# Performance work log

Measured on AMD Instinct MI355X. Metric: run time of the kernel, lower is better.

Reference implementation:

```python
import jax, jax.numpy as jnp
import numpy as np

NUM_HEADS = 12
HEAD_SIZE = 64
B1, B2 = 28, 52          # get_block_sizes(use_dynamic=False): (1456//52, 52)
NUM_FRAMES = 2
SEQ = NUM_FRAMES * B1 * B2   # 2912
BATCH = 1
SCALE = HEAD_SIZE ** -0.5


def _rope(x, cos, sin):
    # interleaved rotary (is_neox_style=False); x [B,T,H,D], cos/sin [T,D//2]
    x1, x2 = x[..., 0::2], x[..., 1::2]
    c, s = cos[:, None, :], sin[:, None, :]
    o1 = x1 * c - x2 * s
    o2 = x2 * c + x1 * s
    return jnp.stack([o1, o2], axis=-1).reshape(x.shape)


def _blin(x, W, b):
    # per-head (batched replicated) linear: x [..., H, Din], W [H, Dout, Din], b [H, Dout]
    return jnp.einsum('...hd,hed->...he', x, W) + b


def _sdpa(q, k, v):
    # q [N,1,H,D], k/v [N,L,H,D] -> [N,1,H,D]
    s = jnp.einsum('nqhd,nkhd->nhqk', q, k) * SCALE
    p = jax.nn.softmax(s, axis=-1)
    return jnp.einsum('nhqk,nkhd->nqhd', p, v)


def _forward(lq, lk, rq, rk, v, cos, sin,
             W_lkq, b_lkq, W_lkk, b_lkk, W_lkv, b_lkv,
             W_rqq, b_rqq, W_rqk, b_rqk, W_rqv, b_rqv):
    B, S, H, D = lq.shape
    F = S // (B1 * B2)
    hd2 = D // 2
    lq_r = _rope(lq, cos, sin).reshape(B, F, B1, B2, H, D)
    # ---- left factor: local attention over b2 within each (frame, b1) block ----
    lkq = lk.reshape(B, F, B1, B2, H, D)[:, :, :, 0]           # [B,F,B1,H,D]
    lkq = _blin(lkq, W_lkq, b_lkq)
    cos_k = cos.reshape(F, B1, B2, hd2)[:, :, 0].reshape(F * B1, hd2)
    sin_k = sin.reshape(F, B1, B2, hd2)[:, :, 0].reshape(F * B1, hd2)
    lkq = _rope(lkq.reshape(B, F * B1, H, D), cos_k, sin_k).reshape(B, F, B1, H, D)
    lkk = _rope(_blin(lk, W_lkk, b_lkk), cos, sin).reshape(B, F, B1, B2, H, D)
    lkv = _blin(lk, W_lkv, b_lkv).reshape(B, F, B1, B2, H, D)
    x = _sdpa(lkq.reshape(-1, 1, H, D), lkk.reshape(-1, B2, H, D), lkv.reshape(-1, B2, H, D))
    lk_out = _rope(x.reshape(B, F * B1, H, D), cos_k, sin_k).reshape(B, F, B1, H, D)
    L = jnp.einsum('baijhd,bfkhd->bhafjik', lq_r, lk_out)      # [B,H,F,F,B2,B1,B1]
    # ---- right factor: local attention over b1 for each (frame, b2) slice ----
    rk_r = _rope(rk, cos, sin).reshape(B, F, B1, B2, H, D)
    rqq = rq.reshape(B, F, B1, B2, H, D)[:, :, 0]              # [B,F,B2,H,D]
    rqq = _blin(rqq, W_rqq, b_rqq)
    cos_j = cos.reshape(F, B1, B2, hd2)[:, 0].reshape(F * B2, hd2)
    sin_j = sin.reshape(F, B1, B2, hd2)[:, 0].reshape(F * B2, hd2)
    rqq = _rope(rqq.reshape(B, F * B2, H, D), cos_j, sin_j).reshape(B, F, B2, H, D)
    rqk = _rope(_blin(rq, W_rqk, b_rqk), cos, sin).reshape(B, F, B1, B2, H, D)
    rqv = _blin(rq, W_rqv, b_rqv).reshape(B, F, B1, B2, H, D)
    kq = jnp.transpose(rqk, (0, 1, 3, 2, 4, 5)).reshape(-1, B1, H, D)  # (b f j) i h d
    vq = jnp.transpose(rqv, (0, 1, 3, 2, 4, 5)).reshape(-1, B1, H, D)
    x = _sdpa(rqq.reshape(-1, 1, H, D), kq, vq)
    rq_out = _rope(x.reshape(B, F * B2, H, D), cos_j, sin_j).reshape(B, F, B2, H, D)
    R = jnp.einsum('bajhd,bfklhd->bhafkjl', rq_out, rk_r)      # [B,H,F,F,B1,B2,B2]
    # ---- combine factors into full logits, softmax, apply to v ----
    out = jnp.einsum('bhafjik,bhafkjl->bhafijkl', L, R)        # [B,H,F,F,B1,B2,B1,B2]
    out = jnp.transpose(out, (0, 1, 2, 4, 5, 3, 6, 7)).reshape(B, H, S, S)
    p = jax.nn.softmax(out * SCALE, axis=-1)
    return jnp.einsum('bhsl,blhd->bshd', p, v)


def setup_inputs() -> dict:
    key = jax.random.key(0)
    ks = jax.random.split(key, 20)
    shp = (BATCH, SEQ, NUM_HEADS, HEAD_SIZE)
    f = lambda k, s: jax.random.normal(k, s, dtype=jnp.float32)
    inp = {'lq': f(ks[0], shp), 'lk': f(ks[1], shp), 'rq': f(ks[2], shp),
           'rk': f(ks[3], shp), 'v': f(ks[4], shp)}
    pos = jnp.arange(SEQ, dtype=jnp.float32)
    inv = 1.0 / (10000.0 ** (jnp.arange(0, HEAD_SIZE, 2, dtype=jnp.float32) / HEAD_SIZE))
    ang = pos[:, None] * inv[None, :]
    inp['cos'], inp['sin'] = jnp.cos(ang), jnp.sin(ang)
    for i, n in enumerate(['lkq', 'lkk', 'lkv', 'rqq', 'rqk', 'rqv']):
        inp['W_' + n] = f(ks[5 + 2 * i], (NUM_HEADS, HEAD_SIZE, HEAD_SIZE)) * (HEAD_SIZE ** -0.5)
        inp['b_' + n] = f(ks[6 + 2 * i], (NUM_HEADS, HEAD_SIZE)) * 0.02
    return inp


def reference(lq, lk, rq, rk, v, cos, sin,
              W_lkq, b_lkq, W_lkk, b_lkk, W_lkv, b_lkv,
              W_rqq, b_rqq, W_rqk, b_rqk, W_rqv, b_rqv):
    return _forward(lq, lk, rq, rk, v, cos, sin,
                    W_lkq, b_lkq, W_lkk, b_lkk, W_lkv, b_lkv,
                    W_rqq, b_rqq, W_rqk, b_rqk, W_rqv, b_rqv)
```

## Files before the change

kernel.cpp:

```cpp
#include <hip/hip_runtime.h>
#include <hip/hip_bf16.h>

#define HH 12
#define DD 64
#define NB1 28
#define NB2 52
#define NF 2
#define FB1 56
#define FB2 104
#define STRIDE_HD 768
#define SCALEF 0.125f

typedef float f32x4 __attribute__((ext_vector_type(4)));
typedef float f32x16 __attribute__((ext_vector_type(16)));
typedef short bf16x8 __attribute__((ext_vector_type(8)));

#if __has_builtin(__builtin_amdgcn_exp2f)
#define EXP2(x) __builtin_amdgcn_exp2f(x)
#else
#define EXP2(x) __expf((x) * 0.6931471805599453f)
#endif

__device__ __forceinline__ unsigned short f2bf(float x) {
  union { float f; unsigned u; } c; c.f = x;
  unsigned r = c.u + 0x7fffu + ((c.u >> 16) & 1u);
  return (unsigned short)(r >> 16);
}
__device__ __forceinline__ float bf2f(unsigned short u) {
  union { unsigned u32v; float f; } c; c.u32v = ((unsigned)u) << 16; return c.f;
}

__global__ __launch_bounds__(256, 4)
void k_proj(const float* __restrict__ lk, const float* __restrict__ rq,
            const float* __restrict__ cosb, const float* __restrict__ sinb,
            const float* __restrict__ W_lkk, const float* __restrict__ b_lkk,
            const float* __restrict__ W_rqk, const float* __restrict__ b_rqk,
            const float* __restrict__ W_lkq, const float* __restrict__ b_lkq,
            const float* __restrict__ W_rqq, const float* __restrict__ b_rqq,
            float* __restrict__ Klg, float* __restrict__ Krg,
            float* __restrict__ ql, float* __restrict__ qr) {
  __shared__ __align__(16) float Wt[64][68];
  __shared__ __align__(16) float xs[64][68];
  __shared__ int srows[64];
  __shared__ int obase[64];

  const int tid = threadIdx.x;
  int bx = blockIdx.x;
  int path, h, c;
  if (bx < 552)       { path = 0; h = bx / 46; c = bx % 46; }
  else if (bx < 1104) { path = 1; bx -= 552;  h = bx / 46; c = bx % 46; }
  else if (bx < 1116) { path = 2; h = bx - 1104; c = 0; }
  else                { path = 3; bx -= 1116; h = bx >> 1; c = bx & 1; }

  const float* X  = (path == 1 || path == 3) ? rq : lk;
  const float* W  = (path == 0) ? W_lkk : (path == 1) ? W_rqk : (path == 2) ? W_lkq : W_rqq;
  const float* bb = (path == 0) ? b_lkk : (path == 1) ? b_rqk : (path == 2) ? b_lkq : b_rqq;
  float* out      = (path == 0) ? Klg : (path == 1) ? Krg : (path == 2) ? ql : qr;
  const int nrows = (path == 0 || path == 1) ? ((c == 45) ? 32 : 64)
                   : (path == 2) ? 56 : ((c == 1) ? 40 : 64);

  for (int idx = tid; idx < 4096; idx += 256)
    Wt[idx & 63][idx >> 6] = W[(size_t)h * 4096 + idx];
  if (tid < 64) {
    int rr = tid, s = 0, ob = 0;
    if (rr < nrows) {
      if (path == 0) {
        s = c * 64 + rr;
        int f = s / 1456, rem = s % 1456, b1 = rem / 52, b2 = rem % 52;
        ob = ((h * 56 + f * 28 + b1) * 52 + b2) * 64;
      } else if (path == 1) {
        s = c * 64 + rr;
        int f = s / 1456, rem = s % 1456, b1 = rem / 52, jj = rem % 52;
        ob = ((h * 104 + f * 52 + jj) * 28 + b1) * 64;
      } else if (path == 2) {
        int q = rr;
        s = (q / 28) * 1456 + (q % 28) * 52;
        ob = (h * 56 + q) * 64;
      } else {
        int q = c * 64 + rr;
        s = (q / 52) * 1456 + (q % 52);
        ob = (h * 104 + q) * 64;
      }
    }
    srows[rr] = s; obase[rr] = ob;
  }
  __syncthreads();
  for (int idx = tid; idx < 4096; idx += 256) {
    int r = idx >> 6, d = idx & 63;
    xs[r][d] = X[(size_t)srows[r] * STRIDE_HD + h * DD + d];
  }
  __syncthreads();

  const int it = tid >> 4, kt = tid & 15;
  f32x4 acc0 = {0,0,0,0}, acc1 = {0,0,0,0}, acc2 = {0,0,0,0}, acc3 = {0,0,0,0};
  #pragma unroll 4
  for (int d4 = 0; d4 < 16; ++d4) {
    f32x4 x0 = *(const f32x4*)&xs[4 * it][4 * d4];
    f32x4 x1 = *(const f32x4*)&xs[4 * it + 1][4 * d4];
    f32x4 x2 = *(const f32x4*)&xs[4 * it + 2][4 * d4];
    f32x4 x3 = *(const f32x4*)&xs[4 * it + 3][4 * d4];
    #pragma unroll
    for (int dd = 0; dd < 4; ++dd) {
      f32x4 wv = *(const f32x4*)&Wt[4 * d4 + dd][4 * kt];
      acc0 += x0[dd] * wv;
      acc1 += x1[dd] * wv;
      acc2 += x2[dd] * wv;
      acc3 += x3[dd] * wv;
    }
  }

  f32x4 bv;
  bv[0] = bb[h * 64 + 4 * kt];     bv[1] = bb[h * 64 + 4 * kt + 1];
  bv[2] = bb[h * 64 + 4 * kt + 2]; bv[3] = bb[h * 64 + 4 * kt + 3];
  #pragma unroll
  for (int rr = 0; rr < 4; ++rr) {
    int row = 4 * it + rr;
    if (row < nrows) {
      f32x4 o = (rr == 0) ? acc0 : (rr == 1) ? acc1 : (rr == 2) ? acc2 : acc3;
      o += bv;
      int s = srows[row];
      float c0 = cosb[s * 32 + 2 * kt],     s0 = sinb[s * 32 + 2 * kt];
      float c1 = cosb[s * 32 + 2 * kt + 1], s1 = sinb[s * 32 + 2 * kt + 1];
      f32x4 res;
      res[0] = o[0] * c0 - o[1] * s0;
      res[1] = o[1] * c0 + o[0] * s0;
      res[2] = o[2] * c1 - o[3] * s1;
      res[3] = o[3] * c1 + o[2] * s1;
      *(f32x4*)(out + obase[row] + 4 * kt) = res;
    }
  }
}

struct SvShared {
  union {
    struct { float qv[64]; float sc[64]; float ps[64]; float ys[64]; float oe[64]; } s;
    float tile[52][68];
  } u;
};

template<int NK, int NG, int GD, int GMUL, int KSTR>
__device__ void sdpa_path(int n, int h, const float* __restrict__ X,
                          const float* __restrict__ Kg, const float* __restrict__ qb,
                          const float* __restrict__ cosb, const float* __restrict__ sinb,
                          const float* __restrict__ Wv, const float* __restrict__ bvv,
                          float* __restrict__ outb, SvShared& sm) {
  const int t = threadIdx.x;
  const int f = n / GD, g = n % GD;
  const int s_base = f * (NB1 * NB2) + g * GMUL;

  if (t < 64) sm.u.s.qv[t] = qb[(size_t)(h * NG + n) * 64 + t];
  __syncthreads();

  if (t < NK * 4) {
    int r = t >> 2, part = t & 3;
    const float4* kr = (const float4*)(Kg + ((size_t)(h * NG + n) * NK + r) * 64 + part * 16);
    const float4* q4 = (const float4*)(sm.u.s.qv + part * 16);
    float p = 0.f;
    #pragma unroll
    for (int i = 0; i < 4; ++i) {
      float4 kv = kr[i], qv4 = q4[i];
      p += kv.x * qv4.x + kv.y * qv4.y + kv.z * qv4.z + kv.w * qv4.w;
    }
    p += __shfl_xor(p, 1); p += __shfl_xor(p, 2);
    if (part == 0) sm.u.s.sc[r] = p * SCALEF;
  }
  __syncthreads();

  if (t < 64) {
    float v = (t < NK) ? sm.u.s.sc[t] : -1e30f;
    float mx = v;
    for (int o = 32; o; o >>= 1) mx = fmaxf(mx, __shfl_xor(mx, o));
    float e = (t < NK) ? __expf(v - mx) : 0.f;
    float sum = e;
    for (int o = 32; o; o >>= 1) sum += __shfl_xor(sum, o);
    sm.u.s.ps[t] = (t < NK) ? e / sum : 0.f;
  }
  __syncthreads();

  {
    int d = t >> 2, g4 = t & 3;
    constexpr int RPG = NK / 4;
    float yp = 0.f;
    #pragma unroll 4
    for (int rr = 0; rr < RPG; ++rr) {
      int r = g4 * RPG + rr;
      yp += sm.u.s.ps[r] * X[(size_t)(s_base + r * KSTR) * STRIDE_HD + h * DD + d];
    }
    yp += __shfl_xor(yp, 1); yp += __shfl_xor(yp, 2);
    if (g4 == 0) sm.u.s.ys[d] = yp;
  }
  __syncthreads();

  {
    int e = t >> 2, part = t & 3;
    const float4* wr = (const float4*)(Wv + (size_t)h * 4096 + e * 64 + part * 16);
    const float4* y4 = (const float4*)(sm.u.s.ys + part * 16);
    float p = 0.f;
    #pragma unroll
    for (int i = 0; i < 4; ++i) {
      float4 wv = wr[i], yv = y4[i];
      p += wv.x * yv.x + wv.y * yv.y + wv.z * yv.z + wv.w * yv.w;
    }
    p += __shfl_xor(p, 1); p += __shfl_xor(p, 2);
    if (part == 0) sm.u.s.oe[e] = p + bvv[h * 64 + e];
  }
  __syncthreads();

  if (t < 32) {
    float co = cosb[s_base * 32 + t], si = sinb[s_base * 32 + t];
    float o0 = sm.u.s.oe[2 * t], o1 = sm.u.s.oe[2 * t + 1];
    outb[(size_t)n * STRIDE_HD + h * DD + 2 * t]     = o0 * co - o1 * si;
    outb[(size_t)n * STRIDE_HD + h * DD + 2 * t + 1] = o1 * co + o0 * si;
  }
}

__device__ void vb_path(int fk, int h, const float* __restrict__ v,
                        unsigned short* __restrict__ vb2, SvShared& sm) {
  const int tid = threadIdx.x;
  for (int idx = tid; idx < NB2 * DD; idx += 256) {
    int l = idx >> 6, d = idx & 63;
    sm.u.tile[l][d] = v[(size_t)(fk * NB2 + l) * STRIDE_HD + h * DD + d];
  }
  __syncthreads();
  for (int idx = tid; idx < 512; idx += 256) {
    int l8 = idx >> 6, d = idx & 63;
    unsigned short tmp[8];
    #pragma unroll
    for (int li = 0; li < 8; ++li) {
      int l = l8 * 8 + li;
      tmp[li] = (l < NB2) ? f2bf(sm.u.tile[l][d]) : (unsigned short)0;
    }
    bf16x8* dst = (bf16x8*)(vb2 + (((size_t)(h * FB1 + fk) * 8 + l8) * 64 + d) * 8);
    *dst = *(bf16x8*)tmp;
  }
}

__global__ __launch_bounds__(256)
void k_sv(const float* __restrict__ lk, const float* __restrict__ rq,
          const float* __restrict__ v,
          const float* __restrict__ cosb, const float* __restrict__ sinb,
          const float* __restrict__ Klg, const float* __restrict__ Krg,
          const float* __restrict__ ql, const float* __restrict__ qr,
          const float* __restrict__ W_lkv, const float* __restrict__ b_lkv,
          const float* __restrict__ W_rqv, const float* __restrict__ b_rqv,
          float* __restrict__ lk_out, float* __restrict__ rq_out,
          unsigned short* __restrict__ vb2) {
  __shared__ SvShared sm;
  const int bx = blockIdx.x;
  if (bx < 672) {
    sdpa_path<52, 56, 28, 52, 1>(bx % 56, bx / 56, lk, Klg, ql, cosb, sinb,
                                 W_lkv, b_lkv, lk_out, sm);
  } else if (bx < 1920) {
    int id = bx - 672;
    sdpa_path<28, 104, 52, 1, 52>(id % 104, id / 104, rq, Krg, qr, cosb, sinb,
                                  W_rqv, b_rqv, rq_out, sm);
  } else {
    int id = bx - 1920;
    vb_path(id % 56, id / 56, v, vb2, sm);
  }
}

struct MgL { unsigned short Yhi[64][64];  unsigned short Ylo[64][64];
             unsigned short Xhi[64][64];  unsigned short Xlo[64][64]; };
struct MgR { unsigned short Yhi[128][64]; unsigned short Ylo[128][64];
             unsigned short Xhi[32][64];  unsigned short Xlo[32][64]; };
union MgShared { MgL L; MgR R; };

__global__ __launch_bounds__(256, 4)
void k_midg(const float* __restrict__ lq, const float* __restrict__ rk,
            const float* __restrict__ lk_out, const float* __restrict__ rq_out,
            const float* __restrict__ cosb, const float* __restrict__ sinb,
            float* __restrict__ LbufN, float* __restrict__ Rbuf) {
  __shared__ __align__(16) MgShared sh;
  const int tid = threadIdx.x;
  const int lane = tid & 63, w = tid >> 6;
  const int hi = lane >> 5, arow = lane & 31;
  int bx = blockIdx.x;

  if (bx < 552) {
    const int h = bx / 46, pt = bx % 46;
    const int rowbase = pt * 64;
    for (int idx = tid; idx < 2048; idx += 256) {
      int q = idx >> 5, m = idx & 31;
      float y0 = 0.f, y1 = 0.f;
      if (q < 56) {
        float2 yv = *(const float2*)(lk_out + (size_t)q * STRIDE_HD + h * DD + 2 * m);
        y0 = yv.x; y1 = yv.y;
      }
      unsigned short h0 = f2bf(y0), h1 = f2bf(y1);
      unsigned short l0 = f2bf(y0 - bf2f(h0)), l1 = f2bf(y1 - bf2f(h1));
      int ms2 = m ^ ((q & 7) << 2);
      ((unsigned*)sh.L.Yhi[q])[ms2] = (unsigned)h0 | ((unsigned)h1 << 16);
      ((unsigned*)sh.L.Ylo[q])[ms2] = (unsigned)l0 | ((unsigned)l1 << 16);
    }
    for (int idx = tid; idx < 2048; idx += 256) {
      int r = idx >> 5, m = idx & 31;
      int srow = rowbase + r;
      float o0 = 0.f, o1 = 0.f;
      if (srow < 2912) {
        float2 xv = *(const float2*)(lq + (size_t)srow * STRIDE_HD + h * DD + 2 * m);
        float co = cosb[srow * 32 + m], si = sinb[srow * 32 + m];
        o0 = xv.x * co - xv.y * si;
        o1 = xv.y * co + xv.x * si;
      }
      unsigned short h0 = f2bf(o0), h1 = f2bf(o1);
      unsigned short l0 = f2bf(o0 - bf2f(h0)), l1 = f2bf(o1 - bf2f(h1));
      int ms2 = m ^ ((r & 7) << 2);
      ((unsigned*)sh.L.Xhi[r])[ms2] = (unsigned)h0 | ((unsigned)h1 << 16);
      ((unsigned*)sh.L.Xlo[r])[ms2] = (unsigned)l0 | ((unsigned)l1 << 16);
    }
    __syncthreads();

    const int xt = w >> 1, qt = w & 1;
    const int brow = qt * 32 + arow;
    const int bswz = (brow & 7) << 3;
    const int xrow = xt * 32 + arow;
    const int aswz = (xrow & 7) << 3;
    f32x16 acc = {0.f,0.f,0.f,0.f,0.f,0.f,0.f,0.f,0.f,0.f,0.f,0.f,0.f,0.f,0.f,0.f};
    #pragma unroll
    for (int ks = 0; ks < 4; ++ks) {
      int kbB = (ks * 16 + hi * 8) ^ bswz;
      int kbA = (ks * 16 + hi * 8) ^ aswz;
      bf16x8 Bhi = *(const bf16x8*)&sh.L.Yhi[brow][kbB];
      bf16x8 Blo = *(const bf16x8*)&sh.L.Ylo[brow][kbB];
      bf16x8 Ahi = *(const bf16x8*)&sh.L.Xhi[xrow][kbA];
      bf16x8 Alo = *(const bf16x8*)&sh.L.Xlo[xrow][kbA];
      acc = __builtin_amdgcn_mfma_f32_32x32x16_bf16(Ahi, Bhi, acc, 0, 0, 0);
      acc = __builtin_amdgcn_mfma_f32_32x32x16_bf16(Ahi, Blo, acc, 0, 0, 0);
      acc = __builtin_amdgcn_mfma_f32_32x32x16_bf16(Alo, Bhi, acc, 0, 0, 0);
    }
    int col = qt * 32 + arow;
    if (col < 56) {
      #pragma unroll
      for (int rg = 0; rg < 16; ++rg) {
        int P = rowbase + xt * 32 + (rg & 3) + 8 * (rg >> 2) + 4 * hi;
        if (P < 2912)
          LbufN[((size_t)h * 2912 + P) * 56 + col] = acc[rg];
      }
    }
  } else {
    bx -= 552;
    const int h = bx / 91, pt = bx % 91;
    const int rowbase = pt * 32;
    for (int idx = tid; idx < 4096; idx += 256) {
      int q = idx >> 5, m = idx & 31;
      float y0 = 0.f, y1 = 0.f;
      if (q < 104) {
        float2 yv = *(const float2*)(rq_out + (size_t)q * STRIDE_HD + h * DD + 2 * m);
        y0 = yv.x; y1 = yv.y;
      }
      unsigned short h0 = f2bf(y0), h1 = f2bf(y1);
      unsigned short l0 = f2bf(y0 - bf2f(h0)), l1 = f2bf(y1 - bf2f(h1));
      int ms2 = m ^ ((q & 7) << 2);
      ((unsigned*)sh.R.Yhi[q])[ms2] = (unsigned)h0 | ((unsigned)h1 << 16);
      ((unsigned*)sh.R.Ylo[q])[ms2] = (unsigned)l0 | ((unsigned)l1 << 16);
    }
    for (int idx = tid; idx < 1024; idx += 256) {
      int r = idx >> 5, m = idx & 31;
      int srow = rowbase + r;
      float2 xv = *(const float2*)(rk + (size_t)srow * STRIDE_HD + h * DD + 2 * m);
      float co = cosb[srow * 32 + m], si = sinb[srow * 32 + m];
      float o0 = xv.x * co - xv.y * si;
      float o1 = xv.y * co + xv.x * si;
      unsigned short h0 = f2bf(o0), h1 = f2bf(o1);
      unsigned short l0 = f2bf(o0 - bf2f(h0)), l1 = f2bf(o1 - bf2f(h1));
      int ms2 = m ^ ((r & 7) << 2);
      ((unsigned*)sh.R.Xhi[r])[ms2] = (unsigned)h0 | ((unsigned)h1 << 16);
      ((unsigned*)sh.R.Xlo[r])[ms2] = (unsigned)l0 | ((unsigned)l1 << 16);
    }
    __syncthreads();

    const int brow = w * 32 + arow;
    const int bswz = (brow & 7) << 3;
    const int aswz = (arow & 7) << 3;
    f32x16 acc = {0.f,0.f,0.f,0.f,0.f,0.f,0.f,0.f,0.f,0.f,0.f,0.f,0.f,0.f,0.f,0.f};
    #pragma unroll
    for (int ks = 0; ks < 4; ++ks) {
      int kbB = (ks * 16 + hi * 8) ^ bswz;
      int kbA = (ks * 16 + hi * 8) ^ aswz;
      bf16x8 Bhi = *(const bf16x8*)&sh.R.Yhi[brow][kbB];
      bf16x8 Blo = *(const bf16x8*)&sh.R.Ylo[brow][kbB];
      bf16x8 Ahi = *(const bf16x8*)&sh.R.Xhi[arow][kbA];
      bf16x8 Alo = *(const bf16x8*)&sh.R.Xlo[arow][kbA];
      acc = __builtin_amdgcn_mfma_f32_32x32x16_bf16(Ahi, Bhi, acc, 0, 0, 0);
      acc = __builtin_amdgcn_mfma_f32_32x32x16_bf16(Ahi, Blo, acc, 0, 0, 0);
      acc = __builtin_amdgcn_mfma_f32_32x32x16_bf16(Alo, Bhi, acc, 0, 0, 0);
    }
    int cq = w * 32 + arow;
    if (cq < 104) {
      int aa = (cq >= 52) ? 1 : 0;
      int jj = cq - aa * 52;
      float* rowp = Rbuf + ((size_t)((h * 2 + aa) * 52 + jj)) * 2912 + rowbase + 4 * hi;
      #pragma unroll
      for (int q4 = 0; q4 < 4; ++q4) {
        f32x4 res = {acc[4 * q4], acc[4 * q4 + 1], acc[4 * q4 + 2], acc[4 * q4 + 3]};
        *(f32x4*)(rowp + 8 * q4) = res;
      }
    }
  }
}

__device__ __forceinline__ bf16x8 make_p8(float Lv, float nm, float4 ra, float4 rb,
                                          int ks, int hi, float& lsum) {
  float p0 = EXP2(fmaf(Lv, ra.x, nm));
  float p1 = EXP2(fmaf(Lv, ra.y, nm));
  float p2 = EXP2(fmaf(Lv, ra.z, nm));
  float p3 = EXP2(fmaf(Lv, ra.w, nm));
  float p4 = EXP2(fmaf(Lv, rb.x, nm));
  float p5 = EXP2(fmaf(Lv, rb.y, nm));
  float p6 = EXP2(fmaf(Lv, rb.z, nm));
  float p7 = EXP2(fmaf(Lv, rb.w, nm));
  if (ks == 3) {
    if (hi == 0) { p4 = 0.f; p5 = 0.f; p6 = 0.f; p7 = 0.f; }
    else { p0 = 0.f; p1 = 0.f; p2 = 0.f; p3 = 0.f;
           p4 = 0.f; p5 = 0.f; p6 = 0.f; p7 = 0.f; }
  }
  lsum += ((p0 + p1) + (p2 + p3)) + ((p4 + p5) + (p6 + p7));
  union { bf16x8 v8; __hip_bfloat162 h2[4]; } pk;
  pk.h2[0] = __float22bfloat162_rn(make_float2(p0, p1));
  pk.h2[1] = __float22bfloat162_rn(make_float2(p2, p3));
  pk.h2[2] = __float22bfloat162_rn(make_float2(p4, p5));
  pk.h2[3] = __float22bfloat162_rn(make_float2(p6, p7));
  return pk.v8;
}

__global__ __launch_bounds__(256, 4)
void k_main(const float* __restrict__ LbufN, const float* __restrict__ Rbuf,
            const unsigned short* __restrict__ vb2, float* __restrict__ outp) {
  const int bid0 = blockIdx.x;
  const int bid = (bid0 & 7) * 156 + (bid0 >> 3);
  const int h = bid / (NF * NB2);
  const int rem = bid % (NF * NB2);
  const int a = rem / NB2, j = rem % NB2;
  const int tid = threadIdx.x;
  const int lane = tid & 63;
  const int w = tid >> 6;
  const int row = lane & 31;
  const int hi = lane >> 5;

  __shared__ __align__(16) union { float Rs[56][64]; float epil[4][16][64]; } ms;
  __shared__ float Rmx[FB1], Rmn[FB1], pmax[4][32], els[4][32];

  const float* Rrow = Rbuf + ((size_t)(h * 2 + a) * 52 + j) * 2912;
  for (int idx = tid; idx < 728; idx += 256) {
    int fk = idx / 13, lc = idx % 13;
    float4 vv = ((const float4*)Rrow)[idx];
    *(float4*)&ms.Rs[fk][lc * 4] = vv;
  }
  __syncthreads();

  if (tid < 224) {
    int fk = tid >> 2, part = tid & 3;
    float mx = -1e30f, mn = 1e30f;
    for (int l = part * 13; l < part * 13 + 13; ++l) {
      float x = ms.Rs[fk][l];
      mx = fmaxf(mx, x); mn = fminf(mn, x);
    }
    mx = fmaxf(mx, __shfl_xor(mx, 1)); mn = fminf(mn, __shfl_xor(mn, 1));
    mx = fmaxf(mx, __shfl_xor(mx, 2)); mn = fminf(mn, __shfl_xor(mn, 2));
    if (part == 0) { Rmx[fk] = mx; Rmn[fk] = mn; }
  }

  const float SC = SCALEF * 1.44269504f;
  float Lv[14];
  {
    const float* Lrow = LbufN + ((size_t)h * 2912 + a * 1456 + row * 52 + j) * 56 + w * 14;
    #pragma unroll
    for (int t = 0; t < 14; ++t)
      Lv[t] = (row < NB1) ? Lrow[t] * SC : 0.f;
  }
  __syncthreads();

  {
    float pm = -1e30f;
    #pragma unroll
    for (int t = 0; t < 14; ++t) {
      int fk = w * 14 + t;
      pm = fmaxf(pm, fmaxf(Lv[t] * Rmx[fk], Lv[t] * Rmn[fk]));
    }
    if (hi == 0) pmax[w][row] = pm;
  }
  __syncthreads();
  const float m2 = fmaxf(fmaxf(pmax[0][row], pmax[1][row]),
                         fmaxf(pmax[2][row], pmax[3][row]));
  const float nm = -m2;

  const bf16x8* vw = (const bf16x8*)vb2 + (size_t)h * 28672 + hi * 64 + row;

  f32x16 acc0 = {0.f,0.f,0.f,0.f,0.f,0.f,0.f,0.f,0.f,0.f,0.f,0.f,0.f,0.f,0.f,0.f};
  f32x16 acc1 = acc0;
  float lsum = 0.f;

  #pragma unroll
  for (int t = 0; t < 14; ++t) {
    const int fk = w * 14 + t;
    const bf16x8* vp = vw + (size_t)fk * 512;
    #pragma unroll
    for (int ks = 0; ks < 4; ++ks) {
      const int k0 = ks * 16 + hi * 8;
      float4 ra = *(const float4*)&ms.Rs[fk][k0];
      float4 rb = *(const float4*)&ms.Rs[fk][k0 + 4];
      bf16x8 pk = make_p8(Lv[t], nm, ra, rb, ks, hi, lsum);
      bf16x8 b0 = vp[ks * 128];
      bf16x8 b1 = vp[ks * 128 + 32];
      acc0 = __builtin_amdgcn_mfma_f32_32x32x16_bf16(pk, b0, acc0, 0, 0, 0);
      acc1 = __builtin_amdgcn_mfma_f32_32x32x16_bf16(pk, b1, acc1, 0, 0, 0);
    }
  }

  lsum += __shfl_xor(lsum, 32);
  if (lane < 32) els[w][lane] = lsum;
  __syncthreads();

  #pragma unroll
  for (int half = 0; half < 2; ++half) {
    if (half) __syncthreads();
    #pragma unroll
    for (int r = 0; r < 16; ++r)
      ms.epil[w][r][lane] = half ? acc1[r] : acc0[r];
    __syncthreads();
    #pragma unroll
    for (int q = 0; q < 4; ++q) {
      int r = w + q * 4;
      int elane = tid & 63;
      float val = ms.epil[0][r][elane] + ms.epil[1][r][elane]
                + ms.epil[2][r][elane] + ms.epil[3][r][elane];
      int irow = (r & 3) + 8 * (r >> 2) + 4 * (elane >> 5);
      if (irow < NB1) {
        float li = 1.0f / (els[0][irow] + els[1][irow] + els[2][irow] + els[3][irow]);
        int srow = a * (NB1 * NB2) + irow * NB2 + j;
        int d = half * 32 + (elane & 31);
        outp[(size_t)srow * STRIDE_HD + h * DD + d] = val * li;
      }
    }
  }
}

extern "C" void kernel_launch(void* const* d_in, const int* in_sizes, int n_in,
                              void* d_out, int out_size, void* d_ws, size_t ws_size,
                              hipStream_t stream) {
  (void)in_sizes; (void)n_in; (void)out_size; (void)ws_size;
  const float* lq   = (const float*)d_in[0];
  const float* lk   = (const float*)d_in[1];
  const float* rq   = (const float*)d_in[2];
  const float* rk   = (const float*)d_in[3];
  const float* v    = (const float*)d_in[4];
  const float* cosb = (const float*)d_in[5];
  const float* sinb = (const float*)d_in[6];
  const float* W_lkq = (const float*)d_in[7];  const float* b_lkq = (const float*)d_in[8];
  const float* W_lkk = (const float*)d_in[9];  const float* b_lkk = (const float*)d_in[10];
  const float* W_lkv = (const float*)d_in[11]; const float* b_lkv = (const float*)d_in[12];
  const float* W_rqq = (const float*)d_in[13]; const float* b_rqq = (const float*)d_in[14];
  const float* W_rqk = (const float*)d_in[15]; const float* b_rqk = (const float*)d_in[16];
  const float* W_rqv = (const float*)d_in[17]; const float* b_rqv = (const float*)d_in[18];

  float* ws = (float*)d_ws;
  float* lk_out = ws;
  float* rq_out = ws + 43008;
  float* LbufN  = ws + 122880;
  float* Rbuf   = ws + 2079744;
  unsigned short* vb2 = (unsigned short*)(ws + 5713920);
  float* ql     = ws + 7090176;
  float* qr     = ws + 7133184;
  float* Klg = LbufN;
  float* Krg = LbufN + 2236416;

  k_proj<<<1140, 256, 0, stream>>>(lk, rq, cosb, sinb,
      W_lkk, b_lkk, W_rqk, b_rqk, W_lkq, b_lkq, W_rqq, b_rqq,
      Klg, Krg, ql, qr);
  k_sv<<<2592, 256, 0, stream>>>(lk, rq, v, cosb, sinb, Klg, Krg, ql, qr,
      W_lkv, b_lkv, W_rqv, b_rqv, lk_out, rq_out, vb2);
  k_midg<<<1644, 256, 0, stream>>>(lq, rk, lk_out, rq_out, cosb, sinb, LbufN, Rbuf);
  k_main<<<1248, 256, 0, stream>>>(LbufN, Rbuf, vb2, (float*)d_out);
}
```

Before: 99.51 us.

## Split k_main key range across two blocks and combine partials in new kernel

Each (head, frame, j) block of the main attention kernel is split into two segments over the 56 key frames, doubling the grid to 2496 blocks. Each segment writes unnormalized partial outputs and partial softmax sums to workspace. A new combine kernel adds the two partials and normalizes. The shared max is still computed over all 56 keys, so no rescaling is needed. This raises parallelism and occupancy at the cost of duplicated R loading, extra global traffic and one more kernel launch.

Measured after the change: 115.3 us. +15.9%, slower.

```diff
diff --git a/kernel.cpp b/kernel.cpp
--- a/kernel.cpp
+++ b/kernel.cpp
@@ -426,11 +426,13 @@
 
 __global__ __launch_bounds__(256, 4)
 void k_main(const float* __restrict__ LbufN, const float* __restrict__ Rbuf,
-            const unsigned short* __restrict__ vb2, float* __restrict__ outp) {
+            const unsigned short* __restrict__ vb2,
+            float* __restrict__ pbuf, float* __restrict__ plsum) {
   const int bid0 = blockIdx.x;
-  const int bid = (bid0 & 7) * 156 + (bid0 >> 3);
-  const int h = bid / (NF * NB2);
-  const int rem = bid % (NF * NB2);
+  const int gb = (bid0 & 7) * 312 + (bid0 >> 3);
+  const int pair = gb >> 1, seg = gb & 1;
+  const int h = pair / (NF * NB2);
+  const int rem = pair % (NF * NB2);
   const int a = rem / NB2, j = rem % NB2;
   const int tid = threadIdx.x;
   const int lane = tid & 63;
@@ -462,21 +464,25 @@
   }
 
   const float SC = SCALEF * 1.44269504f;
-  float Lv[14];
+  const bool rv = (row < NB1);
+  const float* Lbase = LbufN + ((size_t)h * 2912 + a * 1456 + row * 52 + j) * 56;
+  float Lv[7];
   {
-    const float* Lrow = LbufN + ((size_t)h * 2912 + a * 1456 + row * 52 + j) * 56 + w * 14;
-    #pragma unroll
-    for (int t = 0; t < 14; ++t)
-      Lv[t] = (row < NB1) ? Lrow[t] * SC : 0.f;
+    const float* Lc = Lbase + seg * 28 + w * 7;
+    #pragma unroll
+    for (int t = 0; t < 7; ++t)
+      Lv[t] = rv ? Lc[t] * SC : 0.f;
   }
   __syncthreads();
 
   {
+    const float* Lm = Lbase + w * 14;
     float pm = -1e30f;
     #pragma unroll
     for (int t = 0; t < 14; ++t) {
       int fk = w * 14 + t;
-      pm = fmaxf(pm, fmaxf(Lv[t] * Rmx[fk], Lv[t] * Rmn[fk]));
+      float Lx = rv ? Lm[t] * SC : 0.f;
+      pm = fmaxf(pm, fmaxf(Lx * Rmx[fk], Lx * Rmn[fk]));
     }
     if (hi == 0) pmax[w][row] = pm;
   }
@@ -492,8 +498,8 @@
   float lsum = 0.f;
 
   #pragma unroll
-  for (int t = 0; t < 14; ++t) {
-    const int fk = w * 14 + t;
+  for (int t = 0; t < 7; ++t) {
+    const int fk = seg * 28 + w * 7 + t;
     const bf16x8* vp = vw + (size_t)fk * 512;
     #pragma unroll
     for (int ks = 0; ks < 4; ++ks) {
@@ -512,6 +518,12 @@
   if (lane < 32) els[w][lane] = lsum;
   __syncthreads();
 
+  if (tid < NB1)
+    plsum[(size_t)(seg * 1248 + pair) * 28 + tid] =
+        (els[0][tid] + els[1][tid]) + (els[2][tid] + els[3][tid]);
+
+  float* pb = pbuf + (size_t)(seg * 1248 + pair) * 1792;
+
   #pragma unroll
   for (int half = 0; half < 2; ++half) {
     if (half) __syncthreads();
@@ -526,13 +538,31 @@
       float val = ms.epil[0][r][elane] + ms.epil[1][r][elane]
                 + ms.epil[2][r][elane] + ms.epil[3][r][elane];
       int irow = (r & 3) + 8 * (r >> 2) + 4 * (elane >> 5);
-      if (irow < NB1) {
-        float li = 1.0f / (els[0][irow] + els[1][irow] + els[2][irow] + els[3][irow]);
-        int srow = a * (NB1 * NB2) + irow * NB2 + j;
-        int d = half * 32 + (elane & 31);
-        outp[(size_t)srow * STRIDE_HD + h * DD + d] = val * li;
-      }
-    }
+      if (irow < NB1)
+        pb[irow * 64 + half * 32 + (elane & 31)] = val;
+    }
+  }
+}
+
+__global__ __launch_bounds__(256)
+void k_comb(const float* __restrict__ pbuf, const float* __restrict__ plsum,
+            float* __restrict__ outp) {
+  const int bid = blockIdx.x;
+  const int h = bid / (NF * NB2);
+  const int rem = bid % (NF * NB2);
+  const int a = rem / NB2, j = rem % NB2;
+  const int tid = threadIdx.x;
+  __shared__ float li[NB1];
+  if (tid < NB1)
+    li[tid] = 1.0f / (plsum[(size_t)bid * 28 + tid]
+                    + plsum[(size_t)(1248 + bid) * 28 + tid]);
+  __syncthreads();
+  const float* p0 = pbuf + (size_t)bid * 1792;
+  const float* p1 = pbuf + (size_t)(1248 + bid) * 1792;
+  for (int idx = tid; idx < 1792; idx += 256) {
+    int irow = idx >> 6, d = idx & 63;
+    int srow = a * (NB1 * NB2) + irow * NB2 + j;
+    outp[(size_t)srow * STRIDE_HD + h * DD + d] = (p0[idx] + p1[idx]) * li[irow];
   }
 }
 
@@ -562,6 +592,8 @@
   unsigned short* vb2 = (unsigned short*)(ws + 5713920);
   float* ql     = ws + 7090176;
   float* qr     = ws + 7133184;
+  float* plsum  = ws + 7213056;
+  float* pbuf   = ws + 7282944;
   float* Klg = LbufN;
   float* Krg = LbufN + 2236416;
 
@@ -571,5 +603,6 @@
   k_sv<<<2592, 256, 0, stream>>>(lk, rq, v, cosb, sinb, Klg, Krg, ql, qr,
       W_lkv, b_lkv, W_rqv, b_rqv, lk_out, rq_out, vb2);
   k_midg<<<1644, 256, 0, stream>>>(lq, rk, lk_out, rq_out, cosb, sinb, LbufN, Rbuf);
-  k_main<<<1248, 256, 0, stream>>>(LbufN, Rbuf, vb2, (float*)d_out);
-}
+  k_main<<<2496, 256, 0, stream>>>(LbufN, Rbuf, vb2, pbuf, plsum);
+  k_comb<<<1248, 256, 0, stream>>>(pbuf, plsum, (float*)d_out);
+}
```
